# Kernel optimization log

Measured on AMD Instinct MI355X. Metric: run time of the kernel, lower is better.

## Reference

```python
import jax, jax.numpy as jnp
import numpy as np

N, CH, H, W = 8, 256, 64, 64
M, K = 4, 256
CG = CH // M  # per-group input channels


def setup_inputs() -> dict:
    key = jax.random.key(0)
    k1, k2 = jax.random.split(key)
    x = jax.random.normal(k1, (N, CH, H, W), dtype=jnp.float32)
    # grouped conv1x1 weight: [m, k, c_g]  (torch layout is [m*k, c_g, 1, 1])
    w = jax.random.normal(k2, (M, K, CG), dtype=jnp.float32) / np.float32(np.sqrt(CG))
    return {"x": x, "w": w}


def reference(x, w):
    n, c, h, wd = x.shape
    m, k, cg = w.shape
    # grouped 1x1 conv == per-group matmul over channels
    xg = x.reshape(n, m, cg, h, wd)
    logit5 = jnp.einsum('nmchw,mkc->nmhwk', xg, w)  # [n, m, h, w, k]
    # OneHotCategoricalStraightThrough.rsample():
    # hard one-hot sample + (probs - stop_grad(probs))
    probs = jax.nn.softmax(logit5, axis=-1)
    idx = jax.random.categorical(jax.random.key(42), logit5, axis=-1)  # [n, m, h, w]
    one_hot = jax.nn.one_hot(idx, k, dtype=logit5.dtype)
    quantized = jax.lax.stop_gradient(one_hot) + probs - jax.lax.stop_gradient(probs)
    code = jnp.argmax(quantized, axis=-1)  # [n, m, h, w]
    q_out = jnp.transpose(quantized, (0, 1, 4, 2, 3)).reshape(n, m * k, h, wd)
    logit = jnp.transpose(logit5, (0, 1, 4, 2, 3)).reshape(n, m * k, h, wd)
    return q_out, code, logit
```

## Files before the change

### kernel.cpp

```cpp
#include <hip/hip_runtime.h>
#include <stdint.h>

#define CODE_OFF  33554432u
#define LOGIT_OFF 33685504u

typedef __attribute__((address_space(1))) const void g_void;
typedef __attribute__((address_space(3))) void l_void;

__device__ __forceinline__ uint32_t rotl32(uint32_t x, int r) {
  return (x << r) | (x >> (32 - r));
}

__device__ __forceinline__ uint32_t tf32_part(uint32_t i) {
  const uint32_t ks1 = 42u;
  const uint32_t ks2 = 0x1BD11BDAu ^ 42u;
  uint32_t x0 = 0u;
  uint32_t x1 = i + ks1;
#define R4(a,b,c,d) \
  x0 += x1; x1 = rotl32(x1,(a)); x1 ^= x0; \
  x0 += x1; x1 = rotl32(x1,(b)); x1 ^= x0; \
  x0 += x1; x1 = rotl32(x1,(c)); x1 ^= x0; \
  x0 += x1; x1 = rotl32(x1,(d)); x1 ^= x0;
  R4(13,15,26,6)   x0 += ks1; x1 += ks2 + 1u;
  R4(17,29,16,24)  x0 += ks2; x1 += 2u;
  R4(13,15,26,6)               x1 += ks1 + 3u;
  R4(17,29,16,24)  x0 += ks1; x1 += ks2 + 4u;
  R4(13,15,26,6)   x0 += ks2; x1 += 5u;
#undef R4
  return x0 ^ x1;
}

__device__ __forceinline__ float bits_to_gumbel(uint32_t bits) {
  uint32_t fb = (bits >> 9) | 0x3f800000u;
  float f = __uint_as_float(fb) - 1.0f;
  float u = (f > 0.0f) ? f : 1.17549435e-38f;
  return -logf(-logf(u));
}

__global__ __launch_bounds__(256, 4)
void mcq_kernel(const float* __restrict__ x, const float* __restrict__ w,
                float* __restrict__ out) {
  __shared__ __align__(16) float x_lds[1024];
  __shared__ __align__(16) float w_lds[4096];

  const int tid = threadIdx.x;
  const int px = tid & 3;
  const int ty = tid >> 2;
  const int bid = blockIdx.x;
  const int nm = bid >> 9;
  const int half = (bid >> 8) & 1;
  const int tile = bid & 255;
  const int hw0 = tile * 16;
  const int m = nm & 3;
  const int plane = nm + 16 * half;

  float* q_out = out;
  float* code_out = out + CODE_OFF;
  float* logit_out = out + LOGIT_OFF;

  {
    const float* xbase = x + (size_t)plane * 262144 + hw0;
    const float* src = xbase + (size_t)(tid >> 2) * 4096 + (tid & 3) * 4;
    float* dst = x_lds + ((tid & ~63) << 2);
    __builtin_amdgcn_global_load_lds((g_void*)src, (l_void*)dst, 16, 0, 0);
  }

  const float* wrow = w + (size_t)m * 256 * 64;
  float4 wr0, wr1;
  {
    const float* wk = wrow + tid * 64;
    wr0 = *(const float4*)(wk + 0);
    wr1 = *(const float4*)(wk + 4);
    w_lds[0 * 256 + tid] = wr0.x; w_lds[1 * 256 + tid] = wr0.y;
    w_lds[2 * 256 + tid] = wr0.z; w_lds[3 * 256 + tid] = wr0.w;
    w_lds[4 * 256 + tid] = wr1.x; w_lds[5 * 256 + tid] = wr1.y;
    w_lds[6 * 256 + tid] = wr1.z; w_lds[7 * 256 + tid] = wr1.w;
  }
  __syncthreads();

  float acc[4][4], gmb[4][4];
#pragma unroll
  for (int p = 0; p < 4; ++p)
#pragma unroll
    for (int jd = 0; jd < 4; ++jd) acc[p][jd] = 0.0f;

  const uint32_t base0 = ((uint32_t)(plane * 4096 + hw0 + 4 * px)) << 8;

#pragma unroll
  for (int chunk = 0; chunk < 8; ++chunk) {
    if (chunk < 7) {
      const float* wk = wrow + tid * 64 + (chunk + 1) * 8;
      wr0 = *(const float4*)(wk + 0);
      wr1 = *(const float4*)(wk + 4);
    }
    {
#pragma unroll
      for (int i = 0; i < 2; ++i) {
        const int d = chunk * 2 + i;
        const int p = d >> 2, jd = d & 3;
        const uint32_t k = (uint32_t)(ty * 4 + jd);
        gmb[p][jd] = bits_to_gumbel(tf32_part(base0 + (uint32_t)p * 256u + k));
      }
    }
    const int rb = (chunk & 1) << 11;
#pragma unroll
    for (int cc = 0; cc < 8; ++cc) {
      int c = chunk * 8 + cc;
      float4 xv = *(const float4*)&x_lds[c * 16 + px * 4];
      float4 wv = *(const float4*)&w_lds[rb + cc * 256 + ty * 4];
      float xa[4] = {xv.x, xv.y, xv.z, xv.w};
      float wa[4] = {wv.x, wv.y, wv.z, wv.w};
#pragma unroll
      for (int p = 0; p < 4; ++p)
#pragma unroll
        for (int jd = 0; jd < 4; ++jd) acc[p][jd] += xa[p] * wa[jd];
    }
    if (chunk < 7) {
      const int wb = ((chunk + 1) & 1) << 11;
      w_lds[wb + 0 * 256 + tid] = wr0.x; w_lds[wb + 1 * 256 + tid] = wr0.y;
      w_lds[wb + 2 * 256 + tid] = wr0.z; w_lds[wb + 3 * 256 + tid] = wr0.w;
      w_lds[wb + 4 * 256 + tid] = wr1.x; w_lds[wb + 5 * 256 + tid] = wr1.y;
      w_lds[wb + 6 * 256 + tid] = wr1.z; w_lds[wb + 7 * 256 + tid] = wr1.w;
      __syncthreads();
    }
  }

  float best[4]; int ib[4];
#pragma unroll
  for (int p = 0; p < 4; ++p) { best[p] = -3.4e38f; ib[p] = 0; }
  const size_t row_off = (size_t)hw0 + 4 * px;
#pragma unroll
  for (int jd = 0; jd < 4; ++jd) {
    int k = ty * 4 + jd;
    size_t off = ((size_t)(plane * 256 + k)) * 4096 + row_off;
    *(float4*)(logit_out + off) =
        make_float4(acc[0][jd], acc[1][jd], acc[2][jd], acc[3][jd]);
#pragma unroll
    for (int p = 0; p < 4; ++p) {
      float v = gmb[p][jd] + acc[p][jd];
      if (v > best[p]) { best[p] = v; ib[p] = k; }
    }
  }

  __syncthreads();
  float* red_val = w_lds;
  int* red_idx = (int*)(w_lds + 1056);
#pragma unroll
  for (int p = 0; p < 4; ++p) {
    int slot = px * 4 + p;
    red_val[slot * 65 + ty] = best[p];
    red_idx[slot * 65 + ty] = ib[p];
  }
  __syncthreads();
  float* pv = w_lds + 2112;
  int* pi = (int*)(w_lds + 2176);
  if (tid < 64) {
    int slot = tid >> 2, q = tid & 3;
    float bv = -3.4e38f; int bi = 0x7fffffff;
#pragma unroll
    for (int t = 0; t < 16; ++t) {
      float v = red_val[slot * 65 + q * 16 + t];
      int ix = red_idx[slot * 65 + q * 16 + t];
      if (v > bv || (v == bv && ix < bi)) { bv = v; bi = ix; }
    }
    pv[slot * 4 + q] = bv; pi[slot * 4 + q] = bi;
  }
  __syncthreads();
  int* idx_final = (int*)x_lds;
  if (tid < 16) {
    float bv = -3.4e38f; int bi = 0x7fffffff;
#pragma unroll
    for (int q = 0; q < 4; ++q) {
      float v = pv[tid * 4 + q]; int ix = pi[tid * 4 + q];
      if (v > bv || (v == bv && ix < bi)) { bv = v; bi = ix; }
    }
    idx_final[tid] = bi;
    code_out[(size_t)plane * 4096 + hw0 + tid] = (float)bi;
  }
  __syncthreads();

  const int f0 = idx_final[px * 4 + 0];
  const int f1 = idx_final[px * 4 + 1];
  const int f2 = idx_final[px * 4 + 2];
  const int f3 = idx_final[px * 4 + 3];
#pragma unroll
  for (int jd = 0; jd < 4; ++jd) {
    int k = ty * 4 + jd;
    size_t off = ((size_t)(plane * 256 + k)) * 4096 + row_off;
    *(float4*)(q_out + off) = make_float4(k == f0 ? 1.0f : 0.0f, k == f1 ? 1.0f : 0.0f,
                                          k == f2 ? 1.0f : 0.0f, k == f3 ? 1.0f : 0.0f);
  }
}

extern "C" void kernel_launch(void* const* d_in, const int* in_sizes, int n_in,
                              void* d_out, int out_size, void* d_ws, size_t ws_size,
                              hipStream_t stream) {
  const float* x = (const float*)d_in[0];
  const float* w = (const float*)d_in[1];
  float* out = (float*)d_out;
  mcq_kernel<<<dim3(8192), dim3(256), 0, stream>>>(x, w, out);
}
```

Before: 406.4 us.

## Enlarge per-thread register tile to 8x8 and cover both batch halves per block

Each block now handles 32 pixels from two batch planes, one per half, sharing the same weight group, and each thread computes an 8x8 output tile instead of 4x4. This cuts the grid from 8192 to 2048 blocks so each weight tile is loaded and staged once for four times as many outputs. The Gumbel noise is now generated after the matmul instead of interleaved with it, and the index reduction drops to a single shared-memory pass. The larger tile raises register pressure under the 256x4 launch bounds and may cause spills or lower occupancy.

New measurement: 442.4 us. 8.8% more time.

```diff
diff --git a/kernel.cpp b/kernel.cpp
--- a/kernel.cpp
+++ b/kernel.cpp
@@ -40,29 +40,38 @@
 __global__ __launch_bounds__(256, 4)
 void mcq_kernel(const float* __restrict__ x, const float* __restrict__ w,
                 float* __restrict__ out) {
-  __shared__ __align__(16) float x_lds[1024];
+  __shared__ __align__(16) float x_lds[4096];
   __shared__ __align__(16) float w_lds[4096];
 
   const int tid = threadIdx.x;
-  const int px = tid & 3;
-  const int ty = tid >> 2;
+  const int tx = tid & 7;
+  const int ty = tid >> 3;
+  const int half = tx >> 2;
+  const int px = tx & 3;
   const int bid = blockIdx.x;
-  const int nm = bid >> 9;
-  const int half = (bid >> 8) & 1;
-  const int tile = bid & 255;
-  const int hw0 = tile * 16;
+  const int nm = bid >> 7;
+  const int tile = bid & 127;
+  const int hw0 = tile * 32;
+  const int n = nm >> 2;
   const int m = nm & 3;
-  const int plane = nm + 16 * half;
 
   float* q_out = out;
   float* code_out = out + CODE_OFF;
   float* logit_out = out + LOGIT_OFF;
 
   {
-    const float* xbase = x + (size_t)plane * 262144 + hw0;
-    const float* src = xbase + (size_t)(tid >> 2) * 4096 + (tid & 3) * 4;
-    float* dst = x_lds + ((tid & ~63) << 2);
-    __builtin_amdgcn_global_load_lds((g_void*)src, (l_void*)dst, 16, 0, 0);
+    const float* xA = x + (size_t)(n * 256 + m * 64) * 4096 + hw0;
+    const float* xB = xA + (size_t)4 * 256 * 4096;
+#pragma unroll
+    for (int it = 0; it < 4; ++it) {
+      int idx = it * 256 + tid;
+      int c = idx >> 4;
+      int hs = (idx >> 3) & 1;
+      int ck = idx & 7;
+      const float* src = (hs ? xB : xA) + (size_t)c * 4096 + ck * 4;
+      float* dst = x_lds + ((it * 256 + (tid & ~63)) << 2);
+      __builtin_amdgcn_global_load_lds((g_void*)src, (l_void*)dst, 16, 0, 0);
+    }
   }
 
   const float* wrow = w + (size_t)m * 256 * 64;
@@ -78,13 +87,11 @@
   }
   __syncthreads();
 
-  float acc[4][4], gmb[4][4];
-#pragma unroll
-  for (int p = 0; p < 4; ++p)
-#pragma unroll
-    for (int jd = 0; jd < 4; ++jd) acc[p][jd] = 0.0f;
-
-  const uint32_t base0 = ((uint32_t)(plane * 4096 + hw0 + 4 * px)) << 8;
+  float acc[8][8];
+#pragma unroll
+  for (int p = 0; p < 8; ++p)
+#pragma unroll
+    for (int jd = 0; jd < 8; ++jd) acc[p][jd] = 0.0f;
 
 #pragma unroll
   for (int chunk = 0; chunk < 8; ++chunk) {
@@ -93,27 +100,20 @@
       wr0 = *(const float4*)(wk + 0);
       wr1 = *(const float4*)(wk + 4);
     }
-    {
-#pragma unroll
-      for (int i = 0; i < 2; ++i) {
-        const int d = chunk * 2 + i;
-        const int p = d >> 2, jd = d & 3;
-        const uint32_t k = (uint32_t)(ty * 4 + jd);
-        gmb[p][jd] = bits_to_gumbel(tf32_part(base0 + (uint32_t)p * 256u + k));
-      }
-    }
     const int rb = (chunk & 1) << 11;
 #pragma unroll
     for (int cc = 0; cc < 8; ++cc) {
       int c = chunk * 8 + cc;
-      float4 xv = *(const float4*)&x_lds[c * 16 + px * 4];
-      float4 wv = *(const float4*)&w_lds[rb + cc * 256 + ty * 4];
-      float xa[4] = {xv.x, xv.y, xv.z, xv.w};
-      float wa[4] = {wv.x, wv.y, wv.z, wv.w};
-#pragma unroll
-      for (int p = 0; p < 4; ++p)
-#pragma unroll
-        for (int jd = 0; jd < 4; ++jd) acc[p][jd] += xa[p] * wa[jd];
+      float4 xv0 = *(const float4*)&x_lds[c * 64 + half * 32 + px * 8];
+      float4 xv1 = *(const float4*)&x_lds[c * 64 + half * 32 + px * 8 + 4];
+      float4 wv0 = *(const float4*)&w_lds[rb + cc * 256 + ty * 4];
+      float4 wv1 = *(const float4*)&w_lds[rb + cc * 256 + 128 + ty * 4];
+      float xa[8] = {xv0.x, xv0.y, xv0.z, xv0.w, xv1.x, xv1.y, xv1.z, xv1.w};
+      float wa[8] = {wv0.x, wv0.y, wv0.z, wv0.w, wv1.x, wv1.y, wv1.z, wv1.w};
+#pragma unroll
+      for (int p = 0; p < 8; ++p)
+#pragma unroll
+        for (int jd = 0; jd < 8; ++jd) acc[p][jd] += xa[p] * wa[jd];
     }
     if (chunk < 7) {
       const int wb = ((chunk + 1) & 1) << 11;
@@ -125,71 +125,73 @@
     }
   }
 
-  float best[4]; int ib[4];
-#pragma unroll
-  for (int p = 0; p < 4; ++p) { best[p] = -3.4e38f; ib[p] = 0; }
-  const size_t row_off = (size_t)hw0 + 4 * px;
-#pragma unroll
-  for (int jd = 0; jd < 4; ++jd) {
-    int k = ty * 4 + jd;
-    size_t off = ((size_t)(plane * 256 + k)) * 4096 + row_off;
-    *(float4*)(logit_out + off) =
-        make_float4(acc[0][jd], acc[1][jd], acc[2][jd], acc[3][jd]);
-#pragma unroll
-    for (int p = 0; p < 4; ++p) {
-      float v = gmb[p][jd] + acc[p][jd];
-      if (v > best[p]) { best[p] = v; ib[p] = k; }
-    }
-  }
-
-  __syncthreads();
-  float* red_val = w_lds;
-  int* red_idx = (int*)(w_lds + 1056);
-#pragma unroll
-  for (int p = 0; p < 4; ++p) {
-    int slot = px * 4 + p;
-    red_val[slot * 65 + ty] = best[p];
-    red_idx[slot * 65 + ty] = ib[p];
-  }
-  __syncthreads();
-  float* pv = w_lds + 2112;
-  int* pi = (int*)(w_lds + 2176);
+  const int plane = nm + 16 * half;
+  const size_t row_off = (size_t)hw0 + px * 8;
+  const uint32_t base0 = ((uint32_t)(plane * 4096 + hw0 + px * 8)) << 8;
+  float best[8]; int ib[8];
+#pragma unroll
+  for (int p = 0; p < 8; ++p) { best[p] = -3.4e38f; ib[p] = 0; }
+#pragma unroll
+  for (int g = 0; g < 2; ++g)
+#pragma unroll
+    for (int d = 0; d < 4; ++d) {
+      const int jd = g * 4 + d;
+      const int k = g * 128 + ty * 4 + d;
+      size_t off = ((size_t)(plane * 256 + k)) * 4096 + row_off;
+      *(float4*)(logit_out + off) =
+          make_float4(acc[0][jd], acc[1][jd], acc[2][jd], acc[3][jd]);
+      *(float4*)(logit_out + off + 4) =
+          make_float4(acc[4][jd], acc[5][jd], acc[6][jd], acc[7][jd]);
+#pragma unroll
+      for (int p = 0; p < 8; ++p) {
+        float v = bits_to_gumbel(tf32_part(base0 + (uint32_t)(p * 256 + k))) +
+                  acc[p][jd];
+        if (v > best[p]) { best[p] = v; ib[p] = k; }
+      }
+    }
+
+  __syncthreads();
+  float* red_val = x_lds;
+  int* red_idx = (int*)w_lds;
+#pragma unroll
+  for (int p = 0; p < 8; ++p) {
+    int slot = half * 32 + px * 8 + p;
+    red_val[slot * 33 + ty] = best[p];
+    red_idx[slot * 33 + ty] = ib[p];
+  }
+  __syncthreads();
+  int* idx_final = (int*)x_lds + 2112;
   if (tid < 64) {
-    int slot = tid >> 2, q = tid & 3;
     float bv = -3.4e38f; int bi = 0x7fffffff;
 #pragma unroll
-    for (int t = 0; t < 16; ++t) {
-      float v = red_val[slot * 65 + q * 16 + t];
-      int ix = red_idx[slot * 65 + q * 16 + t];
+    for (int t = 0; t < 32; ++t) {
+      float v = red_val[tid * 33 + t];
+      int ix = red_idx[tid * 33 + t];
       if (v > bv || (v == bv && ix < bi)) { bv = v; bi = ix; }
     }
-    pv[slot * 4 + q] = bv; pi[slot * 4 + q] = bi;
-  }
-  __syncthreads();
-  int* idx_final = (int*)x_lds;
-  if (tid < 16) {
-    float bv = -3.4e38f; int bi = 0x7fffffff;
-#pragma unroll
-    for (int q = 0; q < 4; ++q) {
-      float v = pv[tid * 4 + q]; int ix = pi[tid * 4 + q];
-      if (v > bv || (v == bv && ix < bi)) { bv = v; bi = ix; }
-    }
     idx_final[tid] = bi;
-    code_out[(size_t)plane * 4096 + hw0 + tid] = (float)bi;
-  }
-  __syncthreads();
-
-  const int f0 = idx_final[px * 4 + 0];
-  const int f1 = idx_final[px * 4 + 1];
-  const int f2 = idx_final[px * 4 + 2];
-  const int f3 = idx_final[px * 4 + 3];
-#pragma unroll
-  for (int jd = 0; jd < 4; ++jd) {
-    int k = ty * 4 + jd;
-    size_t off = ((size_t)(plane * 256 + k)) * 4096 + row_off;
-    *(float4*)(q_out + off) = make_float4(k == f0 ? 1.0f : 0.0f, k == f1 ? 1.0f : 0.0f,
-                                          k == f2 ? 1.0f : 0.0f, k == f3 ? 1.0f : 0.0f);
-  }
+    int h = tid >> 5;
+    int pos = tid & 31;
+    code_out[(size_t)(nm + 16 * h) * 4096 + hw0 + pos] = (float)bi;
+  }
+  __syncthreads();
+
+  int f[8];
+#pragma unroll
+  for (int p = 0; p < 8; ++p) f[p] = idx_final[half * 32 + px * 8 + p];
+#pragma unroll
+  for (int g = 0; g < 2; ++g)
+#pragma unroll
+    for (int d = 0; d < 4; ++d) {
+      const int k = g * 128 + ty * 4 + d;
+      size_t off = ((size_t)(plane * 256 + k)) * 4096 + row_off;
+      *(float4*)(q_out + off) =
+          make_float4(k == f[0] ? 1.0f : 0.0f, k == f[1] ? 1.0f : 0.0f,
+                      k == f[2] ? 1.0f : 0.0f, k == f[3] ? 1.0f : 0.0f);
+      *(float4*)(q_out + off + 4) =
+          make_float4(k == f[4] ? 1.0f : 0.0f, k == f[5] ? 1.0f : 0.0f,
+                      k == f[6] ? 1.0f : 0.0f, k == f[7] ? 1.0f : 0.0f);
+    }
 }
 
 extern "C" void kernel_launch(void* const* d_in, const int* in_sizes, int n_in,
@@ -198,5 +200,5 @@
   const float* x = (const float*)d_in[0];
   const float* w = (const float*)d_in[1];
   float* out = (float*)d_out;
-  mcq_kernel<<<dim3(8192), dim3(256), 0, stream>>>(x, w, out);
-}
+  mcq_kernel<<<dim3(2048), dim3(256), 0, stream>>>(x, w, out);
+}
```
